# Performance work log

Hardware: AMD Instinct MI355X
Metric: run time of the kernel (lower is better)

The kernel has to match this reference:

```python
import jax, jax.numpy as jnp
import numpy as np

NH, NKV, HD = 4, 2, 128  # heads, kv heads, head_dim (intermediate=512)
EPS = 1e-6


def _lstm(x, Wi, Wh, b):
    # x: (N, S, in) -> (N, S, H); flax OptimizedLSTMCell gate order i,f,g,o
    N = x.shape[0]
    H = Wh.shape[0]
    xz = jnp.einsum('nsi,ij->nsj', x, Wi) + b  # precompute input projection

    def step(carry, z_x):
        c, h = carry
        z = z_x + h @ Wh
        i, f, g, o = jnp.split(z, 4, axis=-1)
        c = jax.nn.sigmoid(f) * c + jax.nn.sigmoid(i) * jnp.tanh(g)
        h = jax.nn.sigmoid(o) * jnp.tanh(c)
        return (c, h), h

    init = (jnp.zeros((N, H), x.dtype), jnp.zeros((N, H), x.dtype))
    _, hs = jax.lax.scan(step, init, jnp.swapaxes(xz, 0, 1))
    return jnp.swapaxes(hs, 0, 1)


def _layernorm(x, scale, bias):
    mu = jnp.mean(x, axis=-1, keepdims=True)
    var = jnp.var(x, axis=-1, keepdims=True)
    return (x - mu) * jax.lax.rsqrt(var + EPS) * scale + bias


def _qk_norm(x, scale):
    mu = jnp.mean(x, axis=-1, keepdims=True)
    var = jnp.var(x, axis=-1, keepdims=True)
    return (x - mu) * jax.lax.rsqrt(var + EPS) * scale


def setup_inputs() -> dict:
    key = jax.random.key(0)
    ks = jax.random.split(key, 12)
    F_in, H = 256, 512  # in_features(=time=features), intermediate
    s = lambda fi: 1.0 / np.sqrt(fi)
    return {
        'series': jax.random.normal(ks[0], (16, 8, 256, 256), jnp.float32),
        'Wi': jax.random.normal(ks[1], (F_in, 4 * H), jnp.float32) * s(F_in),
        'Wh': jax.random.normal(ks[2], (H, 4 * H), jnp.float32) * s(H),
        'b': jnp.zeros((4 * H,), jnp.float32),
        'ln_scale': jnp.ones((H,), jnp.float32),
        'ln_bias': jnp.zeros((H,), jnp.float32),
        'Wq': jax.random.normal(ks[3], (H, NH * HD), jnp.float32) * s(H),
        'Wk': jax.random.normal(ks[4], (H, NKV * HD), jnp.float32) * s(H),
        'Wv': jax.random.normal(ks[5], (H, NKV * HD), jnp.float32) * s(H),
        'qn_scale': jnp.ones((HD,), jnp.float32),
        'kn_scale': jnp.ones((HD,), jnp.float32),
        'Wo': jax.random.normal(ks[6], (NH * HD, H), jnp.float32) * s(NH * HD),
        'Wdown': jax.random.normal(ks[7], (H, F_in), jnp.float32) * s(H),
    }


def reference(series, Wi, Wh, b, ln_scale, ln_bias, Wq, Wk, Wv,
              qn_scale, kn_scale, Wo, Wdown):
    B, D, T, F = series.shape
    # rearrange 'b d h t -> (b d) t h': scan over last axis, axis-2 is step feature
    flat = jnp.swapaxes(series.reshape(B * D, T, F), 1, 2)  # (BD, F, T)
    hid = _lstm(flat, Wi, Wh, b)                             # (BD, F, H)
    H = hid.shape[-1]
    hid = hid.reshape(B, D, T, H)                            # valid since T == F

    # device mixer: GQA over the devices axis
    normed = _layernorm(hid, ln_scale, ln_bias)
    x2 = normed.transpose(0, 2, 1, 3).reshape(B * T, D, H)   # '(b t) d h'
    q = _qk_norm((x2 @ Wq).reshape(B * T, D, NH, HD), qn_scale)
    k = _qk_norm((x2 @ Wk).reshape(B * T, D, NKV, HD), kn_scale)
    v = (x2 @ Wv).reshape(B * T, D, NKV, HD)
    rep = NH // NKV
    k = jnp.repeat(k, rep, axis=2)
    v = jnp.repeat(v, rep, axis=2)
    scores = jnp.einsum('nqhd,nkhd->nhqk', q, k) / np.sqrt(HD).astype(np.float32)
    attn = jax.nn.softmax(scores, axis=-1)
    o = jnp.einsum('nhqk,nkhd->nqhd', attn, v).reshape(B * T, D, NH * HD) @ Wo
    mix = o.reshape(B, T, D, H).transpose(0, 2, 1, 3)

    belief = (hid + mix) @ Wdown                             # (B, D, T, F)
    return belief
```

## Files before the change

kernel.cpp:

```cpp
#include <hip/hip_runtime.h>

typedef unsigned short ushort_t;
typedef __attribute__((ext_vector_type(8))) short bf16x8;
typedef __attribute__((ext_vector_type(4))) float f32x4;

#define DEV __device__ __forceinline__

DEV ushort_t f2bf(float x) {
  union { float f; unsigned u; } v; v.f = x;
  unsigned r = v.u + 0x7fffu + ((v.u >> 16) & 1u);
  return (ushort_t)(r >> 16);
}
DEV float bf2f(ushort_t b) {
  union { unsigned u; float f; } v; v.u = ((unsigned)b) << 16; return v.f;
}
DEV float sigf(float x) { return 1.f / (1.f + __expf(-x)); }

#define OFF_WIT   0x0u
#define OFF_WHT   0x100000u
#define OFF_QKVT  0x300000u
#define OFF_WOT   0x400000u
#define OFF_WDT   0x480000u
#define OFF_BP    0x4C0000u
#define OFF_HB0   0x500000u
#define OFF_HB1   0x520000u
#define OFF_CST   0x540000u
#define OFF_SERT  0x600000u
#define OFF_HID   0x1600000u
#define OFF_NORM  0x3600000u
#define OFF_QB    0x5600000u
#define OFF_KB    0x600000u
#define OFF_VB    0x7600000u
#define OFF_O     0x3600000u
#define OFF_MIX   0x5600000u

__global__ __launch_bounds__(256) void prep_kernel(
    const float* Wi, const float* Wh, const float* Wq, const float* Wk,
    const float* Wv, const float* Wo, const float* Wd, const float* b,
    char* ws) {
  unsigned i = blockIdx.x * 256 + threadIdx.x;
  if (i < 524288u) {
    unsigned j = i >> 8, ii = i & 255u;
    ((ushort_t*)(ws + OFF_WIT))[i] = f2bf(Wi[ii * 2048u + 512u * (j & 3u) + (j >> 2)]);
  } else if (i < 1572864u) {
    unsigned x = i - 524288u; unsigned j = x >> 9, k = x & 511u;
    ((ushort_t*)(ws + OFF_WHT))[x] = f2bf(Wh[(size_t)k * 2048u + 512u * (j & 3u) + (j >> 2)]);
  } else if (i < 2097152u) {
    unsigned x = i - 1572864u; unsigned j = x >> 9, k = x & 511u;
    float v = (j < 512u) ? Wq[k * 512u + j] : (j < 768u) ? Wk[k * 256u + (j - 512u)]
                                                          : Wv[k * 256u + (j - 768u)];
    ((ushort_t*)(ws + OFF_QKVT))[x] = f2bf(v);
  } else if (i < 2359296u) {
    unsigned x = i - 2097152u; unsigned j = x >> 9, k = x & 511u;
    ((ushort_t*)(ws + OFF_WOT))[x] = f2bf(Wo[k * 512u + j]);
  } else if (i < 2490368u) {
    unsigned x = i - 2359296u; unsigned j = x >> 9, k = x & 511u;
    ((ushort_t*)(ws + OFF_WDT))[x] = f2bf(Wd[k * 256u + j]);
  } else if (i < 2492416u) {
    unsigned x = i - 2490368u;
    ((float*)(ws + OFF_BP))[x] = b[512u * (x & 3u) + (x >> 2)];
  } else if (i < 2623488u) {
    unsigned x = i - 2492416u;
    ((ushort_t*)(ws + OFF_HB0))[x] = 0;
  } else if (i < 2754560u) {
    unsigned x = i - 2623488u;
    ((float*)(ws + OFF_CST))[x] = 0.f;
  }
}

__global__ __launch_bounds__(256) void transpose_kernel(const float* series, ushort_t* sert) {
  __shared__ __align__(16) float tl[64][65];
  int n = blockIdx.x;
  int i0 = (blockIdx.y & 3) * 64, s0 = (blockIdx.y >> 2) * 64;
  int tc = threadIdx.x & 63, tr = threadIdx.x >> 6;
  const float* src = series + (size_t)n * 65536u;
#pragma unroll
  for (int p = 0; p < 16; ++p) {
    int r = p * 4 + tr;
    tl[r][tc] = src[(size_t)(i0 + r) * 256u + s0 + tc];
  }
  __syncthreads();
  ushort_t* dst = sert + (size_t)n * 65536u;
#pragma unroll
  for (int p = 0; p < 16; ++p) {
    int sr = p * 4 + tr;
    dst[(size_t)(s0 + sr) * 256u + i0 + tc] = f2bf(tl[tc][sr]);
  }
}

template <int K, int NTOT, int MODE>
__global__ __launch_bounds__(256) void gemm_kernel(
    const ushort_t* A, const ushort_t* BT, const float* bias,
    ushort_t* outb, ushort_t* ob1, ushort_t* ob2, float* outf,
    const ushort_t* Ahid, const ushort_t* Amix, int t0) {
  __shared__ __align__(16) unsigned char smem[128 * 512];
  const int tid = threadIdx.x;
  const int m0 = blockIdx.x * 64;
  const int j0 = blockIdx.y * 64;
  const int w = tid >> 6, l = tid & 63;
  const int lo16 = l & 15, hi4 = l >> 4;
  f32x4 acc[4];
#pragma unroll
  for (int s = 0; s < 4; ++s) acc[s] = (f32x4)(0.f);

  for (int kt = 0; kt < K / 256; ++kt) {
#pragma unroll
    for (int it = 0; it < 16; ++it) {
      int ci = it * 256 + tid;
      int r = ci >> 5, cb = ci & 31;
      bf16x8 val;
      if (MODE == 3 && r < 64) {
        int m = m0 + r;
        int bb = m >> 11, dd = (m >> 8) & 7, tt = m & 255;
        int n2 = ((bb << 8) + tt) * 8 + dd;
        const ushort_t* hp = Ahid + (size_t)m * 512u + kt * 256 + cb * 8;
        const ushort_t* mp = Amix + (size_t)n2 * 512u + kt * 256 + cb * 8;
#pragma unroll
        for (int j = 0; j < 8; ++j) val[j] = (short)f2bf(bf2f(hp[j]) + bf2f(mp[j]));
      } else if (r < 64) {
        val = *(const bf16x8*)(A + (size_t)(m0 + r) * K + kt * 256 + cb * 8);
      } else {
        val = *(const bf16x8*)(BT + (size_t)(j0 + (r - 64)) * K + kt * 256 + cb * 8);
      }
      int rr = r & 63;
      unsigned char* base = smem + ((r < 64) ? 0 : 64 * 512);
      *(bf16x8*)(base + rr * 512 + ((cb * 16) ^ ((rr & 7) << 4))) = val;
    }
    __syncthreads();

    const unsigned char* As = smem;
    const unsigned char* Bs = smem + 64 * 512;
    const int rB = 16 * w + lo16;
    const unsigned char* bbase = Bs + rB * 512;
    const int bswz = (rB & 7) << 4;
    const int aswz = (lo16 & 7) << 4;
#pragma unroll
    for (int kk = 0; kk < 256; kk += 32) {
      const int kb = kk * 2 + hi4 * 16;
      bf16x8 bf = *(const bf16x8*)(bbase + (kb ^ bswz));
#pragma unroll
      for (int s = 0; s < 4; ++s) {
        const int rA = 16 * s + lo16;
        bf16x8 af = *(const bf16x8*)(As + rA * 512 + (kb ^ aswz));
        acc[s] = __builtin_amdgcn_mfma_f32_16x16x32_bf16(af, bf, acc[s], 0, 0, 0);
      }
    }
    __syncthreads();
  }

  const int col = j0 + 16 * w + lo16;
#pragma unroll
  for (int s = 0; s < 4; ++s) {
#pragma unroll
    for (int jj = 0; jj < 4; ++jj) {
      int m = m0 + 16 * s + hi4 * 4 + jj;
      float v = acc[s][jj];
      if (MODE == 1) {
        if (col < 512) outb[(size_t)m * 512u + col] = f2bf(v);
        else if (col < 768) ob1[(size_t)m * 256u + (col - 512)] = f2bf(v);
        else ob2[(size_t)m * 256u + (col - 768)] = f2bf(v);
      } else if (MODE == 2) {
        outb[(size_t)m * NTOT + col] = f2bf(v);
      } else {
        outf[(size_t)m * NTOT + col] = v;
      }
    }
  }
}

__global__ __launch_bounds__(256, 1) void lstm_step3_kernel(
    const ushort_t* hp, ushort_t* hn, float* cst, const ushort_t* wht,
    const ushort_t* wit, const float* bp, const ushort_t* sert,
    ushort_t* hidb, int t) {
  const int tid = threadIdx.x;
  const int n0 = blockIdx.x * 64;
  const int j0 = blockIdx.y * 16;
  const int w = tid >> 6, l = tid & 63;
  const int lo16 = l & 15, hi4 = l >> 4;
  const int row = n0 + w * 16 + lo16;
  const int colA = j0 + lo16;

  const ushort_t* hrow = hp + (size_t)row * 512u + hi4 * 8;
  const ushort_t* xrow = sert + (size_t)row * 65536u + (size_t)t * 256u + hi4 * 8;
  const ushort_t* wh_p = wht + (size_t)colA * 512u + hi4 * 8;
  const ushort_t* wi_p = wit + (size_t)colA * 256u + hi4 * 8;

  f32x4 acc = (f32x4)(0.f);
#pragma unroll
  for (int i = 0; i < 16; ++i) {
    bf16x8 af = *(const bf16x8*)(wh_p + i * 32);
    bf16x8 bf = *(const bf16x8*)(hrow + i * 32);
    acc = __builtin_amdgcn_mfma_f32_16x16x32_bf16(af, bf, acc, 0, 0, 0);
  }
#pragma unroll
  for (int i = 0; i < 8; ++i) {
    bf16x8 af = *(const bf16x8*)(wi_p + i * 32);
    bf16x8 bf = *(const bf16x8*)(xrow + i * 32);
    acc = __builtin_amdgcn_mfma_f32_16x16x32_bf16(af, bf, acc, 0, 0, 0);
  }

  const int u = (j0 >> 2) + hi4;
  const float4 b4 = *(const float4*)(bp + j0 + 4 * hi4);
  const size_t ci = (size_t)row * 512u + u;
  float c = cst[ci];
  float ig = sigf(acc[0] + b4.x);
  float fg = sigf(acc[1] + b4.y);
  float gg = tanhf(acc[2] + b4.z);
  float og = sigf(acc[3] + b4.w);
  c = fg * c + ig * gg;
  cst[ci] = c;
  float h = og * tanhf(c);
  ushort_t hb16 = f2bf(h);
  hn[ci] = hb16;
  hidb[((size_t)row * 256u + (unsigned)t) * 512u + u] = hb16;
}

__global__ __launch_bounds__(256) void ln_kernel(const ushort_t* hidb, const float* sc,
                                                 const float* bi, ushort_t* normed) {
  int row = blockIdx.x * 4 + (threadIdx.x >> 6);
  int l = threadIdx.x & 63;
  bf16x8 hv = *(const bf16x8*)(hidb + (size_t)row * 512u + l * 8);
  float v[8];
  float s1 = 0.f, s2 = 0.f;
#pragma unroll
  for (int j = 0; j < 8; ++j) {
    v[j] = bf2f((ushort_t)hv[j]);
    s1 += v[j]; s2 += v[j] * v[j];
  }
#pragma unroll
  for (int off = 1; off < 64; off <<= 1) {
    s1 += __shfl_xor(s1, off);
    s2 += __shfl_xor(s2, off);
  }
  float mu = s1 * (1.f / 512.f);
  float var = s2 * (1.f / 512.f) - mu * mu;
  float rs = rsqrtf(var + 1e-6f);
  int bb = row >> 11, dd = (row >> 8) & 7, tt = row & 255;
  int n2 = ((bb << 8) + tt) * 8 + dd;
  bf16x8 o;
#pragma unroll
  for (int j = 0; j < 8; ++j)
    o[j] = (short)f2bf((v[j] - mu) * rs * sc[l * 8 + j] + bi[l * 8 + j]);
  *(bf16x8*)(normed + (size_t)n2 * 512u + l * 8) = o;
}

__global__ __launch_bounds__(256) void attn_kernel(const ushort_t* qb, const ushort_t* kb,
                                                   const ushort_t* vb, const float* qn,
                                                   const float* kn, ushort_t* ob) {
  __shared__ __align__(16) float sm[4][3240];
  const int n = blockIdx.x;
  const int w = threadIdx.x >> 6;
  const int l = threadIdx.x & 63;
  const int dq = l >> 3, c = l & 7;
  float* q_s = &sm[w][0];
  float* k_s = q_s + 1056;
  float* v_s = k_s + 1056;
  float* a_s = v_s + 1056;
  const int hk = w >> 1;

  {
    const ushort_t* src = qb + ((size_t)n * 8u + dq) * 512u + w * 128 + c * 16;
    bf16x8 a0 = *(const bf16x8*)src, a1 = *(const bf16x8*)(src + 8);
    float v[16], s1 = 0.f, s2 = 0.f;
#pragma unroll
    for (int j = 0; j < 16; ++j) {
      v[j] = bf2f((ushort_t)(j < 8 ? a0[j] : a1[j - 8]));
      s1 += v[j]; s2 += v[j] * v[j];
    }
    for (int off = 1; off < 8; off <<= 1) { s1 += __shfl_xor(s1, off); s2 += __shfl_xor(s2, off); }
    float mu = s1 * (1.f / 128.f);
    float rs = rsqrtf(s2 * (1.f / 128.f) - mu * mu + 1e-6f);
#pragma unroll
    for (int j = 0; j < 16; ++j)
      q_s[dq * 132 + c * 16 + j] = (v[j] - mu) * rs * qn[c * 16 + j] * 0.08838834764831845f;
  }
  {
    const ushort_t* src = kb + ((size_t)n * 8u + dq) * 256u + hk * 128 + c * 16;
    bf16x8 a0 = *(const bf16x8*)src, a1 = *(const bf16x8*)(src + 8);
    float v[16], s1 = 0.f, s2 = 0.f;
#pragma unroll
    for (int j = 0; j < 16; ++j) {
      v[j] = bf2f((ushort_t)(j < 8 ? a0[j] : a1[j - 8]));
      s1 += v[j]; s2 += v[j] * v[j];
    }
    for (int off = 1; off < 8; off <<= 1) { s1 += __shfl_xor(s1, off); s2 += __shfl_xor(s2, off); }
    float mu = s1 * (1.f / 128.f);
    float rs = rsqrtf(s2 * (1.f / 128.f) - mu * mu + 1e-6f);
#pragma unroll
    for (int j = 0; j < 16; ++j)
      k_s[dq * 132 + c * 16 + j] = (v[j] - mu) * rs * kn[c * 16 + j];
  }
  {
    const ushort_t* src = vb + ((size_t)n * 8u + dq) * 256u + hk * 128 + c * 16;
    bf16x8 a0 = *(const bf16x8*)src, a1 = *(const bf16x8*)(src + 8);
#pragma unroll
    for (int j = 0; j < 16; ++j)
      v_s[dq * 132 + c * 16 + j] = bf2f((ushort_t)(j < 8 ? a0[j] : a1[j - 8]));
  }
  __syncthreads();

  float scv = 0.f;
#pragma unroll 16
  for (int i = 0; i < 128; ++i) scv += q_s[dq * 132 + i] * k_s[c * 132 + i];
  float mx = scv;
  for (int off = 1; off < 8; off <<= 1) mx = fmaxf(mx, __shfl_xor(mx, off));
  float e = __expf(scv - mx);
  float sum = e;
  for (int off = 1; off < 8; off <<= 1) sum += __shfl_xor(sum, off);
  a_s[dq * 9 + c] = e / sum;
  __syncthreads();

  float o[16];
#pragma unroll
  for (int j = 0; j < 16; ++j) o[j] = 0.f;
#pragma unroll
  for (int dk = 0; dk < 8; ++dk) {
    float a = a_s[dq * 9 + dk];
#pragma unroll
    for (int j = 0; j < 16; ++j) o[j] += a * v_s[dk * 132 + c * 16 + j];
  }
  unsigned* dst = (unsigned*)(ob + ((size_t)n * 8u + dq) * 512u + w * 128 + c * 16);
#pragma unroll
  for (int j = 0; j < 8; ++j)
    dst[j] = (unsigned)f2bf(o[2 * j]) | ((unsigned)f2bf(o[2 * j + 1]) << 16);
}

extern "C" void kernel_launch(void* const* d_in, const int* in_sizes, int n_in,
                              void* d_out, int out_size, void* d_ws, size_t ws_size,
                              hipStream_t stream) {
  const float* series = (const float*)d_in[0];
  const float* Wi = (const float*)d_in[1];
  const float* Wh = (const float*)d_in[2];
  const float* b = (const float*)d_in[3];
  const float* lns = (const float*)d_in[4];
  const float* lnb = (const float*)d_in[5];
  const float* Wq = (const float*)d_in[6];
  const float* Wk = (const float*)d_in[7];
  const float* Wv = (const float*)d_in[8];
  const float* qn = (const float*)d_in[9];
  const float* kn = (const float*)d_in[10];
  const float* Wo = (const float*)d_in[11];
  const float* Wd = (const float*)d_in[12];
  char* ws = (char*)d_ws;

  ushort_t* wit = (ushort_t*)(ws + OFF_WIT);
  ushort_t* wht = (ushort_t*)(ws + OFF_WHT);
  ushort_t* qkvt = (ushort_t*)(ws + OFF_QKVT);
  ushort_t* wot = (ushort_t*)(ws + OFF_WOT);
  ushort_t* wdt = (ushort_t*)(ws + OFF_WDT);
  float* bp = (float*)(ws + OFF_BP);
  ushort_t* hb0 = (ushort_t*)(ws + OFF_HB0);
  ushort_t* hb1 = (ushort_t*)(ws + OFF_HB1);
  float* cst = (float*)(ws + OFF_CST);
  ushort_t* sert = (ushort_t*)(ws + OFF_SERT);
  ushort_t* hidb = (ushort_t*)(ws + OFF_HID);
  ushort_t* normed = (ushort_t*)(ws + OFF_NORM);
  ushort_t* qb = (ushort_t*)(ws + OFF_QB);
  ushort_t* kb = (ushort_t*)(ws + OFF_KB);
  ushort_t* vb = (ushort_t*)(ws + OFF_VB);
  ushort_t* ob = (ushort_t*)(ws + OFF_O);
  ushort_t* mixb = (ushort_t*)(ws + OFF_MIX);

  prep_kernel<<<10760, 256, 0, stream>>>(Wi, Wh, Wq, Wk, Wv, Wo, Wd, b, ws);
  transpose_kernel<<<dim3(128, 16), 256, 0, stream>>>(series, sert);

  for (int t = 0; t < 256; ++t) {
    const ushort_t* hp = (t & 1) ? hb1 : hb0;
    ushort_t* hn = (t & 1) ? hb0 : hb1;
    lstm_step3_kernel<<<dim3(2, 128), 256, 0, stream>>>(
        hp, hn, cst, wht, wit, bp, sert, hidb, t);
  }

  ln_kernel<<<8192, 256, 0, stream>>>(hidb, lns, lnb, normed);

  gemm_kernel<512, 1024, 1><<<dim3(512, 16), 256, 0, stream>>>(
      normed, qkvt, nullptr, qb, kb, vb, nullptr, nullptr, nullptr, 0);

  attn_kernel<<<4096, 256, 0, stream>>>(qb, kb, vb, qn, kn, ob);

  gemm_kernel<512, 512, 2><<<dim3(512, 8), 256, 0, stream>>>(
      ob, wot, nullptr, mixb, nullptr, nullptr, nullptr, nullptr, nullptr, 0);

  gemm_kernel<512, 256, 3><<<dim3(512, 4), 256, 0, stream>>>(
      nullptr, wdt, nullptr, nullptr, nullptr, nullptr, (float*)d_out, hidb, mixb, 0);
}
```

Measured before the change: 2.436 ms.

## Replace per-timestep LSTM launches with one persistent cooperative scan kernel

Replaces 256 separate LSTM step launches with one cooperative kernel that loops over all timesteps. Each block keeps its Wh/Wi weight slices and its cell state in registers, and prefetches the next input row during the step. Blocks that own the same 64-row group synchronise through a per-step atomic counter spin barrier with agent-scope release/acquire fences. This removes per-step launch overhead and repeated weight and state reloads, but depends on all 256 blocks being co-resident, and the bounded spin could silently break ordering if it times out.

```diff
diff --git a/kernel.cpp b/kernel.cpp
--- a/kernel.cpp
+++ b/kernel.cpp
@@ -1,4 +1,5 @@
 #include <hip/hip_runtime.h>
+#include <hip/hip_cooperative_groups.h>
 
 typedef unsigned short ushort_t;
 typedef __attribute__((ext_vector_type(8))) short bf16x8;
@@ -25,6 +26,7 @@
 #define OFF_HB0   0x500000u
 #define OFF_HB1   0x520000u
 #define OFF_CST   0x540000u
+#define OFF_CNT   0x580000u
 #define OFF_SERT  0x600000u
 #define OFF_HID   0x1600000u
 #define OFF_NORM  0x3600000u
@@ -65,6 +67,9 @@
   } else if (i < 2754560u) {
     unsigned x = i - 2623488u;
     ((float*)(ws + OFF_CST))[x] = 0.f;
+  } else if (i < 2755072u) {
+    unsigned x = i - 2754560u;
+    ((unsigned*)(ws + OFF_CNT))[x] = 0u;
   }
 }
 
@@ -168,51 +173,83 @@
   }
 }
 
-__global__ __launch_bounds__(256, 1) void lstm_step3_kernel(
-    const ushort_t* hp, ushort_t* hn, float* cst, const ushort_t* wht,
-    const ushort_t* wit, const float* bp, const ushort_t* sert,
-    ushort_t* hidb, int t) {
+__global__ __launch_bounds__(256, 1) void lstm_scan_kernel(
+    ushort_t* h0, ushort_t* h1, const ushort_t* wht, const ushort_t* wit,
+    const float* bp, const ushort_t* sert, ushort_t* hidb, unsigned* cnt) {
   const int tid = threadIdx.x;
-  const int n0 = blockIdx.x * 64;
-  const int j0 = blockIdx.y * 16;
+  const int blk = blockIdx.x;
+  const int rg = blk >> 7;
+  const int n0 = rg * 64;
+  const int j0 = (blk & 127) * 16;
   const int w = tid >> 6, l = tid & 63;
   const int lo16 = l & 15, hi4 = l >> 4;
   const int row = n0 + w * 16 + lo16;
   const int colA = j0 + lo16;
 
-  const ushort_t* hrow = hp + (size_t)row * 512u + hi4 * 8;
-  const ushort_t* xrow = sert + (size_t)row * 65536u + (size_t)t * 256u + hi4 * 8;
   const ushort_t* wh_p = wht + (size_t)colA * 512u + hi4 * 8;
   const ushort_t* wi_p = wit + (size_t)colA * 256u + hi4 * 8;
-
-  f32x4 acc = (f32x4)(0.f);
-#pragma unroll
-  for (int i = 0; i < 16; ++i) {
-    bf16x8 af = *(const bf16x8*)(wh_p + i * 32);
-    bf16x8 bf = *(const bf16x8*)(hrow + i * 32);
-    acc = __builtin_amdgcn_mfma_f32_16x16x32_bf16(af, bf, acc, 0, 0, 0);
-  }
-#pragma unroll
-  for (int i = 0; i < 8; ++i) {
-    bf16x8 af = *(const bf16x8*)(wi_p + i * 32);
-    bf16x8 bf = *(const bf16x8*)(xrow + i * 32);
-    acc = __builtin_amdgcn_mfma_f32_16x16x32_bf16(af, bf, acc, 0, 0, 0);
-  }
+  bf16x8 wr[16], wir[8];
+#pragma unroll
+  for (int i = 0; i < 16; ++i) wr[i] = *(const bf16x8*)(wh_p + i * 32);
+#pragma unroll
+  for (int i = 0; i < 8; ++i) wir[i] = *(const bf16x8*)(wi_p + i * 32);
 
   const int u = (j0 >> 2) + hi4;
   const float4 b4 = *(const float4*)(bp + j0 + 4 * hi4);
-  const size_t ci = (size_t)row * 512u + u;
-  float c = cst[ci];
-  float ig = sigf(acc[0] + b4.x);
-  float fg = sigf(acc[1] + b4.y);
-  float gg = tanhf(acc[2] + b4.z);
-  float og = sigf(acc[3] + b4.w);
-  c = fg * c + ig * gg;
-  cst[ci] = c;
-  float h = og * tanhf(c);
-  ushort_t hb16 = f2bf(h);
-  hn[ci] = hb16;
-  hidb[((size_t)row * 256u + (unsigned)t) * 512u + u] = hb16;
+  float creg = 0.f;
+  unsigned* mycnt = cnt + rg * 256;
+
+  const ushort_t* hrow0 = h0 + (size_t)row * 512u + hi4 * 8;
+  const ushort_t* hrow1 = h1 + (size_t)row * 512u + hi4 * 8;
+  const ushort_t* xrow = sert + (size_t)row * 65536u + hi4 * 8;
+  ushort_t* hn0 = h0 + (size_t)row * 512u + u;
+  ushort_t* hn1 = h1 + (size_t)row * 512u + u;
+  ushort_t* hidp = hidb + (size_t)row * 131072u + u;
+
+  bf16x8 xf[8];
+#pragma unroll
+  for (int i = 0; i < 8; ++i) xf[i] = *(const bf16x8*)(xrow + i * 32);
+
+  for (int t = 0; t < 256; ++t) {
+    const ushort_t* hr = (t & 1) ? hrow1 : hrow0;
+    f32x4 acc = (f32x4)(0.f);
+#pragma unroll
+    for (int i = 0; i < 16; ++i) {
+      bf16x8 bf = *(const bf16x8*)(hr + i * 32);
+      acc = __builtin_amdgcn_mfma_f32_16x16x32_bf16(wr[i], bf, acc, 0, 0, 0);
+    }
+#pragma unroll
+    for (int i = 0; i < 8; ++i)
+      acc = __builtin_amdgcn_mfma_f32_16x16x32_bf16(wir[i], xf[i], acc, 0, 0, 0);
+
+    float ig = sigf(acc[0] + b4.x);
+    float fg = sigf(acc[1] + b4.y);
+    float gg = tanhf(acc[2] + b4.z);
+    float og = sigf(acc[3] + b4.w);
+    creg = fg * creg + ig * gg;
+    float h = og * tanhf(creg);
+    ushort_t hb16 = f2bf(h);
+    *((t & 1) ? hn0 : hn1) = hb16;
+    hidp[(size_t)t * 512u] = hb16;
+
+    if (t < 255) {
+#pragma unroll
+      for (int i = 0; i < 8; ++i)
+        xf[i] = *(const bf16x8*)(xrow + (size_t)(t + 1) * 256u + i * 32);
+      __builtin_amdgcn_fence(__ATOMIC_RELEASE, "agent");
+      __syncthreads();
+      if (tid == 0) {
+        __hip_atomic_fetch_add(&mycnt[t], 1u, __ATOMIC_RELAXED, __HIP_MEMORY_SCOPE_AGENT);
+        unsigned v; int it = 0;
+        do {
+          v = __hip_atomic_load(&mycnt[t], __ATOMIC_RELAXED, __HIP_MEMORY_SCOPE_AGENT);
+          __builtin_amdgcn_s_sleep(1);
+        } while (v < 128u && ++it < 200000);
+      }
+      __syncthreads();
+      __builtin_amdgcn_fence(__ATOMIC_ACQUIRE, "agent");
+    }
+  }
 }
 
 __global__ __launch_bounds__(256) void ln_kernel(const ushort_t* hidb, const float* sc,
@@ -351,7 +388,7 @@
   float* bp = (float*)(ws + OFF_BP);
   ushort_t* hb0 = (ushort_t*)(ws + OFF_HB0);
   ushort_t* hb1 = (ushort_t*)(ws + OFF_HB1);
-  float* cst = (float*)(ws + OFF_CST);
+  unsigned* cnt = (unsigned*)(ws + OFF_CNT);
   ushort_t* sert = (ushort_t*)(ws + OFF_SERT);
   ushort_t* hidb = (ushort_t*)(ws + OFF_HID);
   ushort_t* normed = (ushort_t*)(ws + OFF_NORM);
@@ -361,15 +398,13 @@
   ushort_t* ob = (ushort_t*)(ws + OFF_O);
   ushort_t* mixb = (ushort_t*)(ws + OFF_MIX);
 
-  prep_kernel<<<10760, 256, 0, stream>>>(Wi, Wh, Wq, Wk, Wv, Wo, Wd, b, ws);
+  prep_kernel<<<10762, 256, 0, stream>>>(Wi, Wh, Wq, Wk, Wv, Wo, Wd, b, ws);
   transpose_kernel<<<dim3(128, 16), 256, 0, stream>>>(series, sert);
 
-  for (int t = 0; t < 256; ++t) {
-    const ushort_t* hp = (t & 1) ? hb1 : hb0;
-    ushort_t* hn = (t & 1) ? hb0 : hb1;
-    lstm_step3_kernel<<<dim3(2, 128), 256, 0, stream>>>(
-        hp, hn, cst, wht, wit, bp, sert, hidb, t);
-  }
+  void* kargs[] = {(void*)&hb0, (void*)&hb1, (void*)&wht, (void*)&wit,
+                   (void*)&bp,  (void*)&sert, (void*)&hidb, (void*)&cnt};
+  hipLaunchCooperativeKernel((void*)lstm_scan_kernel, dim3(256), dim3(256),
+                             kargs, 0, stream);
 
   ln_kernel<<<8192, 256, 0, stream>>>(hidb, lns, lnb, normed);
 
```

After: 9.192 ms. 3.77x slower.
